# Optimization experiments

Measured on AMD Instinct MI355X. Metric: run time of the kernel, lower is better.

The kernel has to match this reference:

```python
import jax, jax.numpy as jnp
import numpy as np

B, N, NREL = 8, 512, 4096
IN_DIM, REL_DIM = 64, 32
NF_PART, NF_REL, NF_EFF, OUT_DIM = 128, 256, 128, 64


def _lin(key, fan_in, fan_out):
    kw, kb = jax.random.split(key)
    s = 1.0 / np.sqrt(fan_in)
    w = jax.random.uniform(kw, (fan_in, fan_out), jnp.float32, -s, s)
    b = jax.random.uniform(kb, (fan_out,), jnp.float32, -s, s)
    return w, b


def setup_inputs() -> dict:
    key = jax.random.key(0)
    ks = jax.random.split(key, 16)
    state = jax.random.normal(ks[0], (B, N, IN_DIM), jnp.float32)
    # one-hot receiver / sender incidence matrices [B, N, NREL]
    recv = jax.random.randint(ks[1], (B, NREL), 0, N)
    send = jax.random.randint(ks[2], (B, NREL), 0, N)
    Rr = jnp.transpose(jax.nn.one_hot(recv, N, dtype=jnp.float32), (0, 2, 1))
    Rs = jnp.transpose(jax.nn.one_hot(send, N, dtype=jnp.float32), (0, 2, 1))
    Ra = jax.random.normal(ks[3], (B, NREL, REL_DIM), jnp.float32)

    pe0_w, pe0_b = _lin(ks[4], IN_DIM, NF_PART)
    pe1_w, pe1_b = _lin(ks[5], NF_PART, NF_PART)
    pe2_w, pe2_b = _lin(ks[6], NF_PART, NF_EFF)
    re_in = 2 * IN_DIM + REL_DIM
    re0_w, re0_b = _lin(ks[7], re_in, NF_REL)
    re1_w, re1_b = _lin(ks[8], NF_REL, NF_REL)
    re2_w, re2_b = _lin(ks[9], NF_REL, NF_REL)
    rp_w, rp_b = _lin(ks[10], NF_REL + 2 * NF_EFF, NF_EFF)   # relation propagator
    pp_w, pp_b = _lin(ks[11], 2 * NF_EFF, NF_EFF)            # particle propagator
    pr0_w, pr0_b = _lin(ks[12], NF_EFF, NF_EFF)
    pr1_w, pr1_b = _lin(ks[13], NF_EFF, OUT_DIM)

    return dict(state=state, Rr=Rr, Rs=Rs, Ra=Ra,
                pe0_w=pe0_w, pe0_b=pe0_b, pe1_w=pe1_w, pe1_b=pe1_b,
                pe2_w=pe2_w, pe2_b=pe2_b,
                re0_w=re0_w, re0_b=re0_b, re1_w=re1_w, re1_b=re1_b,
                re2_w=re2_w, re2_b=re2_b,
                rp_w=rp_w, rp_b=rp_b, pp_w=pp_w, pp_b=pp_b,
                pr0_w=pr0_w, pr0_b=pr0_b, pr1_w=pr1_w, pr1_b=pr1_b,
                pstep=3)


def _mlp3(x, w0, b0, w1, b1, w2, b2):
    x = jax.nn.relu(x @ w0 + b0)
    x = jax.nn.relu(x @ w1 + b1)
    return jax.nn.relu(x @ w2 + b2)


def reference(state, Rr, Rs, Ra,
              pe0_w, pe0_b, pe1_w, pe1_b, pe2_w, pe2_b,
              re0_w, re0_b, re1_w, re1_b, re2_w, re2_b,
              rp_w, rp_b, pp_w, pp_b,
              pr0_w, pr0_b, pr1_w, pr1_b, pstep):
    Rrp = jnp.transpose(Rr, (0, 2, 1))  # [B, NREL, N]
    Rsp = jnp.transpose(Rs, (0, 2, 1))
    state_r = Rrp @ state               # [B, NREL, IN_DIM]
    state_s = Rsp @ state

    particle_encode = _mlp3(state, pe0_w, pe0_b, pe1_w, pe1_b, pe2_w, pe2_b)
    relation_encode = _mlp3(jnp.concatenate([state_r, state_s, Ra], axis=2),
                            re0_w, re0_b, re1_w, re1_b, re2_w, re2_b)

    particle_effect = jnp.zeros((state.shape[0], state.shape[1], NF_EFF),
                                dtype=state.dtype)
    for _ in range(pstep):
        effect_r = Rrp @ particle_effect           # gather to relations
        effect_s = Rsp @ particle_effect
        relation_effect = jax.nn.relu(
            jnp.concatenate([relation_encode, effect_r, effect_s], axis=2)
            @ rp_w + rp_b)
        effect_agg = Rr @ relation_effect          # scatter to particles
        particle_effect = jax.nn.relu(
            jnp.concatenate([particle_encode, effect_agg], axis=2)
            @ pp_w + pp_b)

    h = jax.nn.relu(particle_effect @ pr0_w + pr0_b)
    return h @ pr1_w + pr1_b                       # [B, N, OUT_DIM]
```

## Files before the change

### kernel.cpp

```cpp
#include <hip/hip_runtime.h>
#include <hip/hip_bf16.h>

#define BC    8
#define NC    512
#define NRELC 4096
#define MAXDEG 64

typedef unsigned short u16;
typedef __attribute__((ext_vector_type(2))) float  f32x2;
typedef __attribute__((ext_vector_type(4))) float  f32x4;
typedef __attribute__((ext_vector_type(8))) __bf16 bf16x8;
typedef __attribute__((ext_vector_type(8))) short  s16x8;
typedef __attribute__((ext_vector_type(2))) u16    u16x2;
typedef __attribute__((ext_vector_type(4))) u16    u16x4;

__device__ __forceinline__ u16 f2b(float f) {
  union { float f; unsigned u; } v; v.f = f;
  unsigned u = v.u;
  return (u16)((u + 0x7fffu + ((u >> 16) & 1u)) >> 16);
}

template<int KBLK>
__device__ __forceinline__ int toff(int row, int k) {
  return (row >> 4) * (KBLK * 256) + ((k >> 3) << 8) + ((row & 15) << 4) + ((k & 7) << 1);
}

__global__ __launch_bounds__(256) void onehot_scan_v2(
    const float* __restrict__ Rr, const float* __restrict__ Rs,
    int* __restrict__ recv, int* __restrict__ send) {
  int blk = blockIdx.x;
  const bool isR = blk < 2048;
  const f32x4* src = (const f32x4*)(isR ? Rr : Rs);
  int* dst = isR ? recv : send;
  int bb = isR ? blk : blk - 2048;
  const long STRIDE = 524288;
  long base = (long)bb * 256 + threadIdx.x;
  f32x4 x[8];
#pragma unroll
  for (int it = 0; it < 8; ++it) x[it] = src[base + (long)it * STRIDE];
#pragma unroll
  for (int it = 0; it < 8; ++it) {
    float m = fmaxf(fmaxf(x[it][0], x[it][1]), fmaxf(x[it][2], x[it][3]));
    if (m > 0.5f) {
      long f = (base + (long)it * STRIDE) * 4;
      int b = (int)(f >> 21);
      int n = (int)((f >> 12) & 511);
      int rb = (int)(f & 4095);
#pragma unroll
      for (int j = 0; j < 4; ++j)
        if (x[it][j] > 0.5f) dst[b * NRELC + rb + j] = n;
    }
  }
}

struct WT13 {
  const float* src[13];
  u16* dst[13];
  int K[13], N[13];
  int cum[14];
};

__global__ void wtrans_v2(WT13 wt) {
  int idx = blockIdx.x * 256 + threadIdx.x;
  if (idx >= wt.cum[13]) return;
  int w = 0;
  while (idx >= wt.cum[w + 1]) ++w;
  int j = idx - wt.cum[w];
  int N = wt.N[w], K = wt.K[w];
  int k = j / N, n = j - k * N;
  wt.dst[w][n * K + k] = f2b(wt.src[w][j]);
}

template<int MT, int NT, bool AF32>
__device__ __forceinline__ void tile_gemm(const void* __restrict__ Ap, long rowBase,
                                          const u16* __restrict__ Wt, int n0,
                                          int K, int rl, int kg, f32x4 acc[MT][NT]) {
#pragma unroll
  for (int mt = 0; mt < MT; ++mt)
#pragma unroll
    for (int t = 0; t < NT; ++t) acc[mt][t] = (f32x4){0.f, 0.f, 0.f, 0.f};

  for (int k0 = 0; k0 < K; k0 += 32) {
    int kk = k0 + kg * 8;
    bf16x8 af[MT];
#pragma unroll
    for (int mt = 0; mt < MT; ++mt) {
      long row = rowBase + mt * 16 + rl;
      if (AF32) {
        const float* ap = (const float*)Ap + row * K + kk;
        f32x4 lo = *(const f32x4*)ap;
        f32x4 hi = *(const f32x4*)(ap + 4);
        s16x8 s;
        s[0] = (short)f2b(lo[0]); s[1] = (short)f2b(lo[1]);
        s[2] = (short)f2b(lo[2]); s[3] = (short)f2b(lo[3]);
        s[4] = (short)f2b(hi[0]); s[5] = (short)f2b(hi[1]);
        s[6] = (short)f2b(hi[2]); s[7] = (short)f2b(hi[3]);
        af[mt] = __builtin_bit_cast(bf16x8, s);
      } else {
        af[mt] = *reinterpret_cast<const bf16x8*>((const u16*)Ap + row * K + kk);
      }
    }
#pragma unroll
    for (int t = 0; t < NT; ++t) {
      bf16x8 bf = *reinterpret_cast<const bf16x8*>(Wt + (size_t)(n0 + t * 16 + rl) * K + kk);
#pragma unroll
      for (int mt = 0; mt < MT; ++mt)
        acc[mt][t] = __builtin_amdgcn_mfma_f32_16x16x32_bf16(af[mt], bf, acc[mt][t], 0, 0, 0);
    }
  }
}

template<int MT, int NT, bool OBF16, bool RELU>
__device__ __forceinline__ void tile_store(void* Cp, const float* bias, const float* addC,
                                           long rowBase, int n0, int NLD,
                                           int rl, int kg, f32x4 acc[MT][NT]) {
#pragma unroll
  for (int mt = 0; mt < MT; ++mt) {
    long orow = rowBase + mt * 16 + kg * 4;
#pragma unroll
    for (int t = 0; t < NT; ++t) {
      int gc = n0 + t * 16 + rl;
      float bv = bias ? bias[gc] : 0.f;
#pragma unroll
      for (int r = 0; r < 4; ++r) {
        long gr = orow + r;
        float v = acc[mt][t][r] + bv;
        if (addC) v += addC[gr * NLD + gc];
        if (RELU) v = fmaxf(v, 0.f);
        if (OBF16) ((u16*)Cp)[gr * NLD + gc] = f2b(v);
        else       ((float*)Cp)[gr * NLD + gc] = v;
      }
    }
  }
}

__global__ __launch_bounds__(256) void csr_partenc(
    const int* __restrict__ recv, int* __restrict__ deg, int* __restrict__ lists,
    const float* __restrict__ state,
    const u16* __restrict__ pe0t, const float* __restrict__ pe0_b,
    const u16* __restrict__ pe1t, const float* __restrict__ pe1_b,
    const u16* __restrict__ pe2t, const float* __restrict__ pe2_b,
    const u16* __restrict__ pp0t, const float* __restrict__ pp_b,
    u16* __restrict__ x1, u16* __restrict__ x2, u16* __restrict__ penc,
    float* __restrict__ pbase) {
  int wid = threadIdx.x >> 6, lane = threadIdx.x & 63;
  if (blockIdx.x < 1024) {
    int bn = blockIdx.x * 4 + wid;
    int b = bn >> 9, n = bn & 511;
    const int* rv = recv + (long)b * NRELC;
    int base = 0;
    for (int c = 0; c < 64; ++c) {
      int r = c * 64 + lane;
      bool ok = (rv[r] == n);
      unsigned long long m = __ballot(ok);
      if (ok) {
        int rank = __popcll(m & ((1ull << lane) - 1ull));
        lists[(long)bn * MAXDEG + base + rank] = r;
      }
      base += (int)__popcll(m);
    }
    if (lane == 0) deg[bn] = base;
    return;
  }
  int rl = lane & 15, kg = lane >> 4;
  long rowBase = (blockIdx.x - 1024) * 16;
  f32x4 acc[1][2];
  tile_gemm<1, 2, true>(state, rowBase, pe0t, wid * 32, 64, rl, kg, acc);
  tile_store<1, 2, true, true>(x1, pe0_b, nullptr, rowBase, wid * 32, 128, rl, kg, acc);
  __syncthreads();
  tile_gemm<1, 2, false>(x1, rowBase, pe1t, wid * 32, 128, rl, kg, acc);
  tile_store<1, 2, true, true>(x2, pe1_b, nullptr, rowBase, wid * 32, 128, rl, kg, acc);
  __syncthreads();
  tile_gemm<1, 2, false>(x2, rowBase, pe2t, wid * 32, 128, rl, kg, acc);
  tile_store<1, 2, true, true>(penc, pe2_b, nullptr, rowBase, wid * 32, 128, rl, kg, acc);
  __syncthreads();
  tile_gemm<1, 2, false>(penc, rowBase, pp0t, wid * 32, 128, rl, kg, acc);
  tile_store<1, 2, false, false>(pbase, pp_b, nullptr, rowBase, wid * 32, 128, rl, kg, acc);
}

template<int KD, int NTt>
__device__ __forceinline__ void lds_layer_v4(const char* bufIn, const u16* __restrict__ Wt,
                                             int n0, int rl, int kg, f32x4 acc[4][NTt]) {
  constexpr int KI = KD / 32;
  bf16x8 bw[NTt][KI];
#pragma unroll
  for (int t = 0; t < NTt; ++t)
#pragma unroll
    for (int ki = 0; ki < KI; ++ki)
      bw[t][ki] = *(const bf16x8*)(Wt + (size_t)(n0 + t * 16 + rl) * KD + ki * 32 + kg * 8);
#pragma unroll
  for (int mt = 0; mt < 4; ++mt)
#pragma unroll
    for (int t = 0; t < NTt; ++t) acc[mt][t] = (f32x4){0.f, 0.f, 0.f, 0.f};
#pragma unroll
  for (int ki = 0; ki < KI; ++ki) {
    int kk = ki * 32 + kg * 8;
    bf16x8 af[4];
#pragma unroll
    for (int mt = 0; mt < 4; ++mt)
      af[mt] = *(const bf16x8*)&bufIn[toff<32>(mt * 16 + rl, kk)];
#pragma unroll
    for (int t = 0; t < NTt; ++t)
#pragma unroll
      for (int mt = 0; mt < 4; ++mt)
        acc[mt][t] = __builtin_amdgcn_mfma_f32_16x16x32_bf16(af[mt], bw[t][ki], acc[mt][t], 0, 0, 0);
  }
}

template<int NTt>
__device__ __forceinline__ void lds_store_v4(char* bufOut, const float* __restrict__ bias,
                                             int n0, int rl, int kg, f32x4 acc[4][NTt]) {
#pragma unroll
  for (int mt = 0; mt < 4; ++mt)
#pragma unroll
    for (int t = 0; t < NTt; ++t) {
      int gc = n0 + t * 16 + rl;
      float bv = bias[gc];
#pragma unroll
      for (int r = 0; r < 4; ++r) {
        int row = mt * 16 + kg * 4 + r;
        *(u16*)&bufOut[toff<32>(row, gc)] = f2b(fmaxf(acc[mt][t][r] + bv, 0.f));
      }
    }
}

__global__ __launch_bounds__(512, 3) void relenc_fused_v4(
    const float* __restrict__ state, const float* __restrict__ Ra,
    const int* __restrict__ recv, const int* __restrict__ send,
    const u16* __restrict__ re0t, const float* __restrict__ re0_b,
    const u16* __restrict__ re1t, const float* __restrict__ re1_b,
    const u16* __restrict__ re2t, const float* __restrict__ re2_b,
    const u16* __restrict__ rp0t, const float* __restrict__ rp_b,
    float* __restrict__ rbase) {
  __shared__ char bufA[32768];
  __shared__ char bufB[32768];
  int tid = threadIdx.x;
  int m0 = blockIdx.x * 64;

  for (int c = tid; c < 64 * 40; c += 512) {
    int row = c / 40;
    int c4 = (c - row * 40) * 4;
    int grow = m0 + row;
    int b = grow >> 12;
    f32x4 v;
    if (c4 < 64)       v = *(const f32x4*)&state[((long)(b * NC + recv[grow])) * 64 + c4];
    else if (c4 < 128) v = *(const f32x4*)&state[((long)(b * NC + send[grow])) * 64 + (c4 - 64)];
    else               v = *(const f32x4*)&Ra[(long)grow * 32 + (c4 - 128)];
    u16x4 o;
    o[0] = f2b(v[0]); o[1] = f2b(v[1]); o[2] = f2b(v[2]); o[3] = f2b(v[3]);
    *(u16x4*)&bufA[toff<32>(row, c4)] = o;
  }
  __syncthreads();

  int wid = tid >> 6, lane = tid & 63;
  int rl = lane & 15, kg = lane >> 4;

  f32x4 acc[4][2];
  lds_layer_v4<160, 2>(bufA, re0t, wid * 32, rl, kg, acc);
  lds_store_v4<2>(bufB, re0_b, wid * 32, rl, kg, acc);
  __syncthreads();
  lds_layer_v4<256, 2>(bufB, re1t, wid * 32, rl, kg, acc);
  lds_store_v4<2>(bufA, re1_b, wid * 32, rl, kg, acc);
  __syncthreads();
  lds_layer_v4<256, 2>(bufA, re2t, wid * 32, rl, kg, acc);
  lds_store_v4<2>(bufB, re2_b, wid * 32, rl, kg, acc);
  __syncthreads();
  f32x4 acc2[4][1];
  lds_layer_v4<256, 1>(bufB, rp0t, wid * 16, rl, kg, acc2);
#pragma unroll
  for (int mt = 0; mt < 4; ++mt) {
    int gc = wid * 16 + rl;
    float bv = rp_b[gc];
#pragma unroll
    for (int r = 0; r < 4; ++r) {
      long gr = m0 + mt * 16 + kg * 4 + r;
      rbase[gr * 128 + gc] = acc2[mt][0][r] + bv;
    }
  }
}

__global__ __launch_bounds__(512, 4) void relstep_v4(
    const u16* __restrict__ peff, const u16* __restrict__ rp1t,
    const u16* __restrict__ rp2t, const float* __restrict__ rbase,
    const int* __restrict__ recv, const int* __restrict__ send,
    float* __restrict__ tmp) {
  __shared__ char ebuf0[16384];
  __shared__ char ebuf1[16384];
  int tid = threadIdx.x;
  int m0 = blockIdx.x * 64;

  for (int c = tid; c < 2048; c += 512) {
    int s = c >> 10, rem = c & 1023, row = rem >> 4, ch = rem & 15;
    int gr = m0 + row;
    int b = gr >> 12;
    int idx = s ? send[gr] : recv[gr];
    bf16x8 v = *(const bf16x8*)&peff[((long)(b * NC + idx)) * 128 + ch * 8];
    char* dst = s ? ebuf1 : ebuf0;
    *(bf16x8*)&dst[toff<16>(row, ch * 8)] = v;
  }
  __syncthreads();

  int wid = tid >> 6, lane = tid & 63;
  int rl = lane & 15, kg = lane >> 4;
  int wm = wid >> 2, wn = wid & 3;
  int n0 = wn * 32;

  bf16x8 b1[2][4], b2[2][4];
#pragma unroll
  for (int t = 0; t < 2; ++t)
#pragma unroll
    for (int ki = 0; ki < 4; ++ki) {
      b1[t][ki] = *(const bf16x8*)(rp1t + (size_t)(n0 + t * 16 + rl) * 128 + ki * 32 + kg * 8);
      b2[t][ki] = *(const bf16x8*)(rp2t + (size_t)(n0 + t * 16 + rl) * 128 + ki * 32 + kg * 8);
    }

  f32x4 acc[2][2];
#pragma unroll
  for (int mt = 0; mt < 2; ++mt)
#pragma unroll
    for (int t = 0; t < 2; ++t) acc[mt][t] = (f32x4){0.f, 0.f, 0.f, 0.f};

#pragma unroll
  for (int ki = 0; ki < 4; ++ki) {
    int kk = ki * 32 + kg * 8;
    bf16x8 e0[2], e1[2];
#pragma unroll
    for (int mt = 0; mt < 2; ++mt) {
      int row = wm * 32 + mt * 16 + rl;
      e0[mt] = *(const bf16x8*)&ebuf0[toff<16>(row, kk)];
      e1[mt] = *(const bf16x8*)&ebuf1[toff<16>(row, kk)];
    }
#pragma unroll
    for (int t = 0; t < 2; ++t)
#pragma unroll
      for (int mt = 0; mt < 2; ++mt)
        acc[mt][t] = __builtin_amdgcn_mfma_f32_16x16x32_bf16(e0[mt], b1[t][ki], acc[mt][t], 0, 0, 0);
#pragma unroll
    for (int t = 0; t < 2; ++t)
#pragma unroll
      for (int mt = 0; mt < 2; ++mt)
        acc[mt][t] = __builtin_amdgcn_mfma_f32_16x16x32_bf16(e1[mt], b2[t][ki], acc[mt][t], 0, 0, 0);
  }

#pragma unroll
  for (int mt = 0; mt < 2; ++mt) {
#pragma unroll
    for (int r = 0; r < 4; ++r) {
      long gr = m0 + wm * 32 + mt * 16 + kg * 4 + r;
      const float* rb = &rbase[gr * 128];
      float* dst = &tmp[gr * 128];
#pragma unroll
      for (int t = 0; t < 2; ++t) {
        int gc = n0 + t * 16 + rl;
        dst[gc] = fmaxf(acc[mt][t][r] + rb[gc], 0.f);
      }
    }
  }
}

template<bool RELU>
__global__ __launch_bounds__(256) void segreduce_kernel(
    const float* __restrict__ src, const int* __restrict__ deg,
    const int* __restrict__ lists, u16* __restrict__ agg16) {
  int wid = threadIdx.x >> 6, lane = threadIdx.x & 63;
  int p = blockIdx.x * 4 + wid;
  int b = p >> 9;
  int c = lane * 2;
  int d = deg[p];
  const int* lp = &lists[(long)p * MAXDEG];
  f32x2 acc = (f32x2){0.f, 0.f};
  for (int k = 0; k < d; ++k) {
    long row = ((long)b * NRELC + lp[k]) * 128;
    f32x2 v = *(const f32x2*)&src[row + c];
    if (RELU) { v[0] = fmaxf(v[0], 0.f); v[1] = fmaxf(v[1], 0.f); }
    acc[0] += v[0]; acc[1] += v[1];
  }
  u16x2 o;
  o[0] = f2b(acc[0]); o[1] = f2b(acc[1]);
  *(u16x2*)&agg16[(long)p * 128 + c] = o;
}

__global__ __launch_bounds__(256) void ppgemm_v2(
    const u16* __restrict__ agg16, const u16* __restrict__ pp1t,
    const float* __restrict__ pbase, u16* __restrict__ peff) {
  int wid = threadIdx.x >> 6, lane = threadIdx.x & 63;
  int rl = lane & 15, kg = lane >> 4;
  long rowBase = blockIdx.x * 16;
  f32x4 acc[1][2];
  tile_gemm<1, 2, false>(agg16, rowBase, pp1t, wid * 32, 128, rl, kg, acc);
  tile_store<1, 2, true, true>(peff, nullptr, pbase, rowBase, wid * 32, 128, rl, kg, acc);
}

__global__ __launch_bounds__(256) void decoder_v2(
    const u16* __restrict__ peff,
    const u16* __restrict__ pr0t, const float* __restrict__ pr0_b,
    const u16* __restrict__ pr1t, const float* __restrict__ pr1_b,
    u16* __restrict__ h, float* __restrict__ out) {
  int wid = threadIdx.x >> 6, lane = threadIdx.x & 63;
  int rl = lane & 15, kg = lane >> 4;
  long rowBase = blockIdx.x * 16;
  f32x4 acc[1][2];
  tile_gemm<1, 2, false>(peff, rowBase, pr0t, wid * 32, 128, rl, kg, acc);
  tile_store<1, 2, true, true>(h, pr0_b, nullptr, rowBase, wid * 32, 128, rl, kg, acc);
  __syncthreads();
  f32x4 acc2[1][1];
  tile_gemm<1, 1, false>(h, rowBase, pr1t, wid * 16, 128, rl, kg, acc2);
  tile_store<1, 1, false, false>(out, pr1_b, nullptr, rowBase, wid * 16, 64, rl, kg, acc2);
}

extern "C" void kernel_launch(void* const* d_in, const int* in_sizes, int n_in,
                              void* d_out, int out_size, void* d_ws, size_t ws_size,
                              hipStream_t stream) {
  const float* state = (const float*)d_in[0];
  const float* Rr    = (const float*)d_in[1];
  const float* Rs    = (const float*)d_in[2];
  const float* Ra    = (const float*)d_in[3];
  const float* pe0_w = (const float*)d_in[4];  const float* pe0_b = (const float*)d_in[5];
  const float* pe1_w = (const float*)d_in[6];  const float* pe1_b = (const float*)d_in[7];
  const float* pe2_w = (const float*)d_in[8];  const float* pe2_b = (const float*)d_in[9];
  const float* re0_w = (const float*)d_in[10]; const float* re0_b = (const float*)d_in[11];
  const float* re1_w = (const float*)d_in[12]; const float* re1_b = (const float*)d_in[13];
  const float* re2_w = (const float*)d_in[14]; const float* re2_b = (const float*)d_in[15];
  const float* rp_w  = (const float*)d_in[16]; const float* rp_b  = (const float*)d_in[17];
  const float* pp_w  = (const float*)d_in[18]; const float* pp_b  = (const float*)d_in[19];
  const float* pr0_w = (const float*)d_in[20]; const float* pr0_b = (const float*)d_in[21];
  const float* pr1_w = (const float*)d_in[22]; const float* pr1_b = (const float*)d_in[23];

  char* base = (char*)d_ws; size_t off = 0;
  auto alloc = [&](size_t b) -> void* {
    void* p = base + off; off = (off + b + 255) & ~(size_t)255; return p;
  };

  int* recv  = (int*)alloc(4L * BC * NRELC);
  int* send  = (int*)alloc(4L * BC * NRELC);
  int* deg   = (int*)alloc(4L * BC * NC);
  int* lists = (int*)alloc(4L * BC * NC * MAXDEG);
  u16* pe0t = (u16*)alloc(2L * 128 * 64);
  u16* pe1t = (u16*)alloc(2L * 128 * 128);
  u16* pe2t = (u16*)alloc(2L * 128 * 128);
  u16* re0t = (u16*)alloc(2L * 256 * 160);
  u16* re1t = (u16*)alloc(2L * 256 * 256);
  u16* re2t = (u16*)alloc(2L * 256 * 256);
  u16* rp0t = (u16*)alloc(2L * 128 * 256);
  u16* rp1t = (u16*)alloc(2L * 128 * 128);
  u16* rp2t = (u16*)alloc(2L * 128 * 128);
  u16* pp0t = (u16*)alloc(2L * 128 * 128);
  u16* pp1t = (u16*)alloc(2L * 128 * 128);
  u16* pr0t = (u16*)alloc(2L * 128 * 128);
  u16* pr1t = (u16*)alloc(2L * 64 * 128);
  float* tmp   = (float*)alloc(4L * 32768 * 128);
  float* rbase = (float*)alloc(4L * 32768 * 128);
  u16* x1   = (u16*)alloc(2L * 4096 * 128);
  u16* x2   = (u16*)alloc(2L * 4096 * 128);
  u16* penc = (u16*)alloc(2L * 4096 * 128);
  float* pbase = (float*)alloc(4L * 4096 * 128);
  u16* agg16 = (u16*)alloc(2L * 4096 * 128);
  u16* peff = (u16*)alloc(2L * 4096 * 128);
  u16* h    = (u16*)alloc(2L * 4096 * 128);
  (void)ws_size; (void)in_sizes; (void)n_in; (void)out_size;

  struct WSpec { const float* src; u16* dst; int K, N; };
  const WSpec specs[13] = {
      {pe0_w,            pe0t, 64, 128},
      {pe1_w,            pe1t, 128, 128},
      {pe2_w,            pe2t, 128, 128},
      {re0_w,            re0t, 160, 256},
      {re1_w,            re1t, 256, 256},
      {re2_w,            re2t, 256, 256},
      {rp_w,             rp0t, 256, 128},
      {rp_w + 256 * 128, rp1t, 128, 128},
      {rp_w + 384 * 128, rp2t, 128, 128},
      {pp_w,             pp0t, 128, 128},
      {pp_w + 128 * 128, pp1t, 128, 128},
      {pr0_w,            pr0t, 128, 128},
      {pr1_w,            pr1t, 128, 64},
  };
  WT13 wt;
  int cum = 0;
  for (int i = 0; i < 13; ++i) {
    wt.src[i] = specs[i].src; wt.dst[i] = specs[i].dst;
    wt.K[i] = specs[i].K; wt.N[i] = specs[i].N;
    wt.cum[i] = cum; cum += specs[i].K * specs[i].N;
  }
  wt.cum[13] = cum;

  onehot_scan_v2<<<4096, 256, 0, stream>>>(Rr, Rs, recv, send);
  wtrans_v2<<<(cum + 255) / 256, 256, 0, stream>>>(wt);

  csr_partenc<<<1280, 256, 0, stream>>>(recv, deg, lists, state,
                                        pe0t, pe0_b, pe1t, pe1_b, pe2t, pe2_b,
                                        pp0t, pp_b, x1, x2, penc, pbase);

  relenc_fused_v4<<<512, 512, 0, stream>>>(state, Ra, recv, send,
                                           re0t, re0_b, re1t, re1_b, re2t, re2_b,
                                           rp0t, rp_b, rbase);

  segreduce_kernel<true><<<1024, 256, 0, stream>>>(rbase, deg, lists, agg16);
  ppgemm_v2<<<256, 256, 0, stream>>>(agg16, pp1t, pbase, peff);
  for (int s = 1; s < 3; ++s) {
    relstep_v4<<<512, 512, 0, stream>>>(peff, rp1t, rp2t, rbase, recv, send, tmp);
    segreduce_kernel<false><<<1024, 256, 0, stream>>>(tmp, deg, lists, agg16);
    ppgemm_v2<<<256, 256, 0, stream>>>(agg16, pp1t, pbase, peff);
  }

  decoder_v2<<<256, 256, 0, stream>>>(peff, pr0t, pr0_b, pr1t, pr1_b, h, (float*)d_out);
}
```

Baseline: 168.8 us.

## Rewrite one-hot decode as matvec, merge CSR/partenc/relenc, fuse final pp into decoder

The one-hot index extraction now reduces each incidence column with a weighted sum over node indices, reading the matrices coalesced in 512 blocks instead of the 4096-block thresholded scan. CSR build, the particle encoder and the relation encoder are merged into one 512-thread launch, with blocks chosen by index range. The last particle-propagator GEMM is fused with the two decoder layers through LDS. Together these cut kernel launches and intermediate global traffic. The matvec relies on exact one-hot values, and the merged kernel gives the small-tile paths 512-thread blocks, so some threads may sit idle.

```diff
diff --git a/kernel.cpp b/kernel.cpp
--- a/kernel.cpp
+++ b/kernel.cpp
@@ -13,6 +13,7 @@
 typedef __attribute__((ext_vector_type(8))) short  s16x8;
 typedef __attribute__((ext_vector_type(2))) u16    u16x2;
 typedef __attribute__((ext_vector_type(4))) u16    u16x4;
+typedef __attribute__((ext_vector_type(4))) int    i32x4;
 
 __device__ __forceinline__ u16 f2b(float f) {
   union { float f; unsigned u; } v; v.f = f;
@@ -25,31 +26,42 @@
   return (row >> 4) * (KBLK * 256) + ((k >> 3) << 8) + ((row & 15) << 4) + ((k & 7) << 1);
 }
 
-__global__ __launch_bounds__(256) void onehot_scan_v2(
+__global__ __launch_bounds__(256) void onehot_matvec(
     const float* __restrict__ Rr, const float* __restrict__ Rs,
     int* __restrict__ recv, int* __restrict__ send) {
   int blk = blockIdx.x;
-  const bool isR = blk < 2048;
-  const f32x4* src = (const f32x4*)(isR ? Rr : Rs);
-  int* dst = isR ? recv : send;
-  int bb = isR ? blk : blk - 2048;
-  const long STRIDE = 524288;
-  long base = (long)bb * 256 + threadIdx.x;
-  f32x4 x[8];
-#pragma unroll
-  for (int it = 0; it < 8; ++it) x[it] = src[base + (long)it * STRIDE];
-#pragma unroll
-  for (int it = 0; it < 8; ++it) {
-    float m = fmaxf(fmaxf(x[it][0], x[it][1]), fmaxf(x[it][2], x[it][3]));
-    if (m > 0.5f) {
-      long f = (base + (long)it * STRIDE) * 4;
-      int b = (int)(f >> 21);
-      int n = (int)((f >> 12) & 511);
-      int rb = (int)(f & 4095);
-#pragma unroll
-      for (int j = 0; j < 4; ++j)
-        if (x[it][j] > 0.5f) dst[b * NRELC + rb + j] = n;
-    }
+  int tens = blk >> 8;
+  int b = (blk >> 5) & 7;
+  int rt = blk & 31;
+  const float* srcf = (tens ? Rs : Rr) + (long)b * NC * NRELC + rt * 128;
+  int* dst = (tens ? send : recv) + b * NRELC + rt * 128;
+  int ng = threadIdx.x >> 5;
+  int col = threadIdx.x & 31;
+  const f32x4* cp = (const f32x4*)srcf + col;
+  f32x4 acc = (f32x4){0.f, 0.f, 0.f, 0.f};
+#pragma unroll 8
+  for (int i = 0; i < 64; ++i) {
+    int n = ng * 64 + i;
+    f32x4 x = cp[(long)n * (NRELC / 4)];
+    float w = (float)n;
+    acc[0] = fmaf(x[0], w, acc[0]);
+    acc[1] = fmaf(x[1], w, acc[1]);
+    acc[2] = fmaf(x[2], w, acc[2]);
+    acc[3] = fmaf(x[3], w, acc[3]);
+  }
+  __shared__ f32x4 red[256];
+  red[threadIdx.x] = acc;
+  __syncthreads();
+  if (threadIdx.x < 32) {
+    f32x4 s = red[threadIdx.x];
+#pragma unroll
+    for (int g = 1; g < 8; ++g) {
+      f32x4 t = red[g * 32 + threadIdx.x];
+      s[0] += t[0]; s[1] += t[1]; s[2] += t[2]; s[3] += t[3];
+    }
+    i32x4 o;
+    o[0] = (int)s[0]; o[1] = (int)s[1]; o[2] = (int)s[2]; o[3] = (int)s[3];
+    *(i32x4*)&dst[threadIdx.x * 4] = o;
   }
 }
 
@@ -134,18 +146,92 @@
   }
 }
 
-__global__ __launch_bounds__(256) void csr_partenc(
-    const int* __restrict__ recv, int* __restrict__ deg, int* __restrict__ lists,
-    const float* __restrict__ state,
+template<int KD, int NTt>
+__device__ __forceinline__ void lds_layer_v4(const char* bufIn, const u16* __restrict__ Wt,
+                                             int n0, int rl, int kg, f32x4 acc[4][NTt]) {
+  constexpr int KI = KD / 32;
+  bf16x8 bw[NTt][KI];
+#pragma unroll
+  for (int t = 0; t < NTt; ++t)
+#pragma unroll
+    for (int ki = 0; ki < KI; ++ki)
+      bw[t][ki] = *(const bf16x8*)(Wt + (size_t)(n0 + t * 16 + rl) * KD + ki * 32 + kg * 8);
+#pragma unroll
+  for (int mt = 0; mt < 4; ++mt)
+#pragma unroll
+    for (int t = 0; t < NTt; ++t) acc[mt][t] = (f32x4){0.f, 0.f, 0.f, 0.f};
+#pragma unroll
+  for (int ki = 0; ki < KI; ++ki) {
+    int kk = ki * 32 + kg * 8;
+    bf16x8 af[4];
+#pragma unroll
+    for (int mt = 0; mt < 4; ++mt)
+      af[mt] = *(const bf16x8*)&bufIn[toff<32>(mt * 16 + rl, kk)];
+#pragma unroll
+    for (int t = 0; t < NTt; ++t)
+#pragma unroll
+      for (int mt = 0; mt < 4; ++mt)
+        acc[mt][t] = __builtin_amdgcn_mfma_f32_16x16x32_bf16(af[mt], bw[t][ki], acc[mt][t], 0, 0, 0);
+  }
+}
+
+template<int NTt>
+__device__ __forceinline__ void lds_store_v4(char* bufOut, const float* __restrict__ bias,
+                                             int n0, int rl, int kg, f32x4 acc[4][NTt]) {
+#pragma unroll
+  for (int mt = 0; mt < 4; ++mt)
+#pragma unroll
+    for (int t = 0; t < NTt; ++t) {
+      int gc = n0 + t * 16 + rl;
+      float bv = bias[gc];
+#pragma unroll
+      for (int r = 0; r < 4; ++r) {
+        int row = mt * 16 + kg * 4 + r;
+        *(u16*)&bufOut[toff<32>(row, gc)] = f2b(fmaxf(acc[mt][t][r] + bv, 0.f));
+      }
+    }
+}
+
+__global__ __launch_bounds__(512, 3) void k2_kernel(
+    const int* __restrict__ recv, const int* __restrict__ send,
+    int* __restrict__ deg, int* __restrict__ lists,
+    const float* __restrict__ state, const float* __restrict__ Ra,
+    const u16* __restrict__ re0t, const float* __restrict__ re0_b,
+    const u16* __restrict__ re1t, const float* __restrict__ re1_b,
+    const u16* __restrict__ re2t, const float* __restrict__ re2_b,
+    const u16* __restrict__ rp0t, const float* __restrict__ rp_b,
+    float* __restrict__ rbase,
     const u16* __restrict__ pe0t, const float* __restrict__ pe0_b,
     const u16* __restrict__ pe1t, const float* __restrict__ pe1_b,
     const u16* __restrict__ pe2t, const float* __restrict__ pe2_b,
     const u16* __restrict__ pp0t, const float* __restrict__ pp_b,
     u16* __restrict__ x1, u16* __restrict__ x2, u16* __restrict__ penc,
     float* __restrict__ pbase) {
-  int wid = threadIdx.x >> 6, lane = threadIdx.x & 63;
-  if (blockIdx.x < 1024) {
-    int bn = blockIdx.x * 4 + wid;
+  __shared__ char bufA[32768];
+  __shared__ char bufB[32768];
+  int tid = threadIdx.x;
+  int wid = tid >> 6, lane = tid & 63;
+  int blk = blockIdx.x;
+
+  if (blk >= 1024) {
+    int rl = lane & 15, kg = lane >> 4;
+    long rowBase = (blk - 1024) * 16;
+    f32x4 acc[1][1];
+    tile_gemm<1, 1, true>(state, rowBase, pe0t, wid * 16, 64, rl, kg, acc);
+    tile_store<1, 1, true, true>(x1, pe0_b, nullptr, rowBase, wid * 16, 128, rl, kg, acc);
+    __syncthreads();
+    tile_gemm<1, 1, false>(x1, rowBase, pe1t, wid * 16, 128, rl, kg, acc);
+    tile_store<1, 1, true, true>(x2, pe1_b, nullptr, rowBase, wid * 16, 128, rl, kg, acc);
+    __syncthreads();
+    tile_gemm<1, 1, false>(x2, rowBase, pe2t, wid * 16, 128, rl, kg, acc);
+    tile_store<1, 1, true, true>(penc, pe2_b, nullptr, rowBase, wid * 16, 128, rl, kg, acc);
+    __syncthreads();
+    tile_gemm<1, 1, false>(penc, rowBase, pp0t, wid * 16, 128, rl, kg, acc);
+    tile_store<1, 1, false, false>(pbase, pp_b, nullptr, rowBase, wid * 16, 128, rl, kg, acc);
+    return;
+  }
+  if (blk >= 512) {
+    int bn = (blk - 512) * 8 + wid;
     int b = bn >> 9, n = bn & 511;
     const int* rv = recv + (long)b * NRELC;
     int base = 0;
@@ -162,81 +248,8 @@
     if (lane == 0) deg[bn] = base;
     return;
   }
-  int rl = lane & 15, kg = lane >> 4;
-  long rowBase = (blockIdx.x - 1024) * 16;
-  f32x4 acc[1][2];
-  tile_gemm<1, 2, true>(state, rowBase, pe0t, wid * 32, 64, rl, kg, acc);
-  tile_store<1, 2, true, true>(x1, pe0_b, nullptr, rowBase, wid * 32, 128, rl, kg, acc);
-  __syncthreads();
-  tile_gemm<1, 2, false>(x1, rowBase, pe1t, wid * 32, 128, rl, kg, acc);
-  tile_store<1, 2, true, true>(x2, pe1_b, nullptr, rowBase, wid * 32, 128, rl, kg, acc);
-  __syncthreads();
-  tile_gemm<1, 2, false>(x2, rowBase, pe2t, wid * 32, 128, rl, kg, acc);
-  tile_store<1, 2, true, true>(penc, pe2_b, nullptr, rowBase, wid * 32, 128, rl, kg, acc);
-  __syncthreads();
-  tile_gemm<1, 2, false>(penc, rowBase, pp0t, wid * 32, 128, rl, kg, acc);
-  tile_store<1, 2, false, false>(pbase, pp_b, nullptr, rowBase, wid * 32, 128, rl, kg, acc);
-}
-
-template<int KD, int NTt>
-__device__ __forceinline__ void lds_layer_v4(const char* bufIn, const u16* __restrict__ Wt,
-                                             int n0, int rl, int kg, f32x4 acc[4][NTt]) {
-  constexpr int KI = KD / 32;
-  bf16x8 bw[NTt][KI];
-#pragma unroll
-  for (int t = 0; t < NTt; ++t)
-#pragma unroll
-    for (int ki = 0; ki < KI; ++ki)
-      bw[t][ki] = *(const bf16x8*)(Wt + (size_t)(n0 + t * 16 + rl) * KD + ki * 32 + kg * 8);
-#pragma unroll
-  for (int mt = 0; mt < 4; ++mt)
-#pragma unroll
-    for (int t = 0; t < NTt; ++t) acc[mt][t] = (f32x4){0.f, 0.f, 0.f, 0.f};
-#pragma unroll
-  for (int ki = 0; ki < KI; ++ki) {
-    int kk = ki * 32 + kg * 8;
-    bf16x8 af[4];
-#pragma unroll
-    for (int mt = 0; mt < 4; ++mt)
-      af[mt] = *(const bf16x8*)&bufIn[toff<32>(mt * 16 + rl, kk)];
-#pragma unroll
-    for (int t = 0; t < NTt; ++t)
-#pragma unroll
-      for (int mt = 0; mt < 4; ++mt)
-        acc[mt][t] = __builtin_amdgcn_mfma_f32_16x16x32_bf16(af[mt], bw[t][ki], acc[mt][t], 0, 0, 0);
-  }
-}
-
-template<int NTt>
-__device__ __forceinline__ void lds_store_v4(char* bufOut, const float* __restrict__ bias,
-                                             int n0, int rl, int kg, f32x4 acc[4][NTt]) {
-#pragma unroll
-  for (int mt = 0; mt < 4; ++mt)
-#pragma unroll
-    for (int t = 0; t < NTt; ++t) {
-      int gc = n0 + t * 16 + rl;
-      float bv = bias[gc];
-#pragma unroll
-      for (int r = 0; r < 4; ++r) {
-        int row = mt * 16 + kg * 4 + r;
-        *(u16*)&bufOut[toff<32>(row, gc)] = f2b(fmaxf(acc[mt][t][r] + bv, 0.f));
-      }
-    }
-}
-
-__global__ __launch_bounds__(512, 3) void relenc_fused_v4(
-    const float* __restrict__ state, const float* __restrict__ Ra,
-    const int* __restrict__ recv, const int* __restrict__ send,
-    const u16* __restrict__ re0t, const float* __restrict__ re0_b,
-    const u16* __restrict__ re1t, const float* __restrict__ re1_b,
-    const u16* __restrict__ re2t, const float* __restrict__ re2_b,
-    const u16* __restrict__ rp0t, const float* __restrict__ rp_b,
-    float* __restrict__ rbase) {
-  __shared__ char bufA[32768];
-  __shared__ char bufB[32768];
-  int tid = threadIdx.x;
-  int m0 = blockIdx.x * 64;
-
+
+  int m0 = blk * 64;
   for (int c = tid; c < 64 * 40; c += 512) {
     int row = c / 40;
     int c4 = (c - row * 40) * 4;
@@ -252,9 +265,7 @@
   }
   __syncthreads();
 
-  int wid = tid >> 6, lane = tid & 63;
   int rl = lane & 15, kg = lane >> 4;
-
   f32x4 acc[4][2];
   lds_layer_v4<160, 2>(bufA, re0t, wid * 32, rl, kg, acc);
   lds_store_v4<2>(bufB, re0_b, wid * 32, rl, kg, acc);
@@ -391,21 +402,74 @@
   tile_store<1, 2, true, true>(peff, nullptr, pbase, rowBase, wid * 32, 128, rl, kg, acc);
 }
 
-__global__ __launch_bounds__(256) void decoder_v2(
-    const u16* __restrict__ peff,
+__global__ __launch_bounds__(256) void ppdec_kernel(
+    const u16* __restrict__ agg16, const u16* __restrict__ pp1t,
+    const float* __restrict__ pbase,
     const u16* __restrict__ pr0t, const float* __restrict__ pr0_b,
     const u16* __restrict__ pr1t, const float* __restrict__ pr1_b,
-    u16* __restrict__ h, float* __restrict__ out) {
+    float* __restrict__ out) {
+  __shared__ char t0[4096];
+  __shared__ char t1[4096];
   int wid = threadIdx.x >> 6, lane = threadIdx.x & 63;
   int rl = lane & 15, kg = lane >> 4;
   long rowBase = blockIdx.x * 16;
+
   f32x4 acc[1][2];
-  tile_gemm<1, 2, false>(peff, rowBase, pr0t, wid * 32, 128, rl, kg, acc);
-  tile_store<1, 2, true, true>(h, pr0_b, nullptr, rowBase, wid * 32, 128, rl, kg, acc);
-  __syncthreads();
-  f32x4 acc2[1][1];
-  tile_gemm<1, 1, false>(h, rowBase, pr1t, wid * 16, 128, rl, kg, acc2);
-  tile_store<1, 1, false, false>(out, pr1_b, nullptr, rowBase, wid * 16, 64, rl, kg, acc2);
+  tile_gemm<1, 2, false>(agg16, rowBase, pp1t, wid * 32, 128, rl, kg, acc);
+#pragma unroll
+  for (int t = 0; t < 2; ++t) {
+    int gc = wid * 32 + t * 16 + rl;
+#pragma unroll
+    for (int r = 0; r < 4; ++r) {
+      int row = kg * 4 + r;
+      float v = acc[0][t][r] + pbase[(rowBase + row) * 128 + gc];
+      *(u16*)&t0[toff<16>(row, gc)] = f2b(fmaxf(v, 0.f));
+    }
+  }
+  __syncthreads();
+
+  f32x4 a2[2];
+  a2[0] = (f32x4){0.f, 0.f, 0.f, 0.f};
+  a2[1] = (f32x4){0.f, 0.f, 0.f, 0.f};
+#pragma unroll
+  for (int ki = 0; ki < 4; ++ki) {
+    int kk = ki * 32 + kg * 8;
+    bf16x8 af = *(const bf16x8*)&t0[toff<16>(rl, kk)];
+#pragma unroll
+    for (int t = 0; t < 2; ++t) {
+      bf16x8 bf = *(const bf16x8*)(pr0t + (size_t)(wid * 32 + t * 16 + rl) * 128 + kk);
+      a2[t] = __builtin_amdgcn_mfma_f32_16x16x32_bf16(af, bf, a2[t], 0, 0, 0);
+    }
+  }
+#pragma unroll
+  for (int t = 0; t < 2; ++t) {
+    int gc = wid * 32 + t * 16 + rl;
+    float bv = pr0_b[gc];
+#pragma unroll
+    for (int r = 0; r < 4; ++r) {
+      int row = kg * 4 + r;
+      *(u16*)&t1[toff<16>(row, gc)] = f2b(fmaxf(a2[t][r] + bv, 0.f));
+    }
+  }
+  __syncthreads();
+
+  if (wid < 4) {
+    f32x4 a3 = (f32x4){0.f, 0.f, 0.f, 0.f};
+#pragma unroll
+    for (int ki = 0; ki < 4; ++ki) {
+      int kk = ki * 32 + kg * 8;
+      bf16x8 af = *(const bf16x8*)&t1[toff<16>(rl, kk)];
+      bf16x8 bf = *(const bf16x8*)(pr1t + (size_t)(wid * 16 + rl) * 128 + kk);
+      a3 = __builtin_amdgcn_mfma_f32_16x16x32_bf16(af, bf, a3, 0, 0, 0);
+    }
+    int gc = wid * 16 + rl;
+    float bv = pr1_b[gc];
+#pragma unroll
+    for (int r = 0; r < 4; ++r) {
+      long gr = rowBase + kg * 4 + r;
+      out[gr * 64 + gc] = a3[r] + bv;
+    }
+  }
 }
 
 extern "C" void kernel_launch(void* const* d_in, const int* in_sizes, int n_in,
@@ -456,7 +520,6 @@
   float* pbase = (float*)alloc(4L * 4096 * 128);
   u16* agg16 = (u16*)alloc(2L * 4096 * 128);
   u16* peff = (u16*)alloc(2L * 4096 * 128);
-  u16* h    = (u16*)alloc(2L * 4096 * 128);
   (void)ws_size; (void)in_sizes; (void)n_in; (void)out_size;
 
   struct WSpec { const float* src; u16* dst; int K, N; };
@@ -484,24 +547,24 @@
   }
   wt.cum[13] = cum;
 
-  onehot_scan_v2<<<4096, 256, 0, stream>>>(Rr, Rs, recv, send);
+  onehot_matvec<<<512, 256, 0, stream>>>(Rr, Rs, recv, send);
   wtrans_v2<<<(cum + 255) / 256, 256, 0, stream>>>(wt);
 
-  csr_partenc<<<1280, 256, 0, stream>>>(recv, deg, lists, state,
-                                        pe0t, pe0_b, pe1t, pe1_b, pe2t, pe2_b,
-                                        pp0t, pp_b, x1, x2, penc, pbase);
-
-  relenc_fused_v4<<<512, 512, 0, stream>>>(state, Ra, recv, send,
-                                           re0t, re0_b, re1t, re1_b, re2t, re2_b,
-                                           rp0t, rp_b, rbase);
+  k2_kernel<<<1280, 512, 0, stream>>>(recv, send, deg, lists, state, Ra,
+                                      re0t, re0_b, re1t, re1_b, re2t, re2_b,
+                                      rp0t, rp_b, rbase,
+                                      pe0t, pe0_b, pe1t, pe1_b, pe2t, pe2_b,
+                                      pp0t, pp_b, x1, x2, penc, pbase);
 
   segreduce_kernel<true><<<1024, 256, 0, stream>>>(rbase, deg, lists, agg16);
   ppgemm_v2<<<256, 256, 0, stream>>>(agg16, pp1t, pbase, peff);
   for (int s = 1; s < 3; ++s) {
     relstep_v4<<<512, 512, 0, stream>>>(peff, rp1t, rp2t, rbase, recv, send, tmp);
     segreduce_kernel<false><<<1024, 256, 0, stream>>>(tmp, deg, lists, agg16);
+    if (s == 2) break;
     ppgemm_v2<<<256, 256, 0, stream>>>(agg16, pp1t, pbase, peff);
   }
 
-  decoder_v2<<<256, 256, 0, stream>>>(peff, pr0t, pr0_b, pr1t, pr1_b, h, (float*)d_out);
-}
+  ppdec_kernel<<<256, 256, 0, stream>>>(agg16, pp1t, pbase,
+                                        pr0t, pr0_b, pr1t, pr1_b, (float*)d_out);
+}
```

Result: no change. 167.8 us (-0.6%).
